# Optimization experiments

Hardware: AMD Instinct MI355X
Metric: run time of the kernel (lower is better)

## Reference

```python
import jax, jax.numpy as jnp
import numpy as np

HEADS = 8
WH, WW = 8, 8
DIM = 256
B = 4096
N = WH * WW  # 64


def _rel_index():
    ch, cw = np.meshgrid(np.arange(WH), np.arange(WW), indexing='ij')
    coords = np.stack([ch.ravel(), cw.ravel()])  # (2, N)
    rel = coords[:, :, None] - coords[:, None, :]  # (2, N, N)
    rel = rel.transpose(1, 2, 0)
    rel[:, :, 0] += WH - 1
    rel[:, :, 1] += WW - 1
    rel[:, :, 0] *= 2 * WW - 1
    return jnp.asarray(rel.sum(-1), dtype=jnp.int32)  # (N, N)


def setup_inputs() -> dict:
    key = jax.random.key(0)
    ks = jax.random.split(key, 6)
    x = jax.random.normal(ks[0], (B, N, DIM), dtype=jnp.float32)
    attn_mask = jnp.zeros((1, HEADS, N, N), dtype=jnp.float32)
    w_qkv = jax.random.normal(ks[1], (3 * DIM, DIM), dtype=jnp.float32) * 0.02
    w_proj = jax.random.normal(ks[2], (DIM, DIM), dtype=jnp.float32) * 0.02
    b_proj = jax.random.normal(ks[3], (DIM,), dtype=jnp.float32) * 0.02
    table = jax.random.normal(ks[4], (225, HEADS), dtype=jnp.float32) * 0.02
    return {"x": x, "attn_mask": attn_mask, "w_qkv": w_qkv, "w_proj": w_proj,
            "b_proj": b_proj, "table": table, "rel_index": _rel_index()}


def reference(x, attn_mask, w_qkv, w_proj, b_proj, table, rel_index):
    Bn, Nn, C = x.shape
    hd = C // HEADS
    qkv = (x @ w_qkv.T).reshape(Bn, Nn, 3, HEADS, hd)
    q = qkv[:, :, 0].transpose(0, 2, 1, 3)  # (B,h,N,d)
    k = qkv[:, :, 1].transpose(0, 2, 1, 3)
    v = qkv[:, :, 2].transpose(0, 2, 1, 3)
    scale = 1.0 / jnp.sqrt(jnp.asarray(hd, dtype=x.dtype))
    attn = jnp.einsum('bhnd,bhmd->bhnm', q, k) * scale
    bias = table[rel_index]  # (N,N,h)
    attn = attn + bias.transpose(2, 0, 1)[None] + attn_mask
    attn = jax.nn.softmax(attn, axis=-1)
    out = jnp.einsum('bhnm,bhmd->bhnd', attn, v)
    out = out.transpose(0, 2, 1, 3).reshape(Bn, Nn, C)
    return out @ w_proj.T + b_proj
```

## Files before the change

kernel.cpp:

```cpp
#include <hip/hip_runtime.h>
#include <hip/hip_bf16.h>

#define HEADS 8
#define NTOK 64
#define DIM 256

typedef __attribute__((ext_vector_type(8))) short bf16x8;
typedef __attribute__((ext_vector_type(4))) short bf16x4;
typedef __attribute__((ext_vector_type(4))) float f32x4;
typedef unsigned short u16;

__device__ __forceinline__ u16 f2bf(float f) {
    union { float f; unsigned u; } c; c.f = f;
    unsigned u = c.u;
    unsigned rounded = u + 0x7FFF + ((u >> 16) & 1);
    return (u16)(rounded >> 16);
}

__global__ void prep_kernel(const float* __restrict__ wqkv,
                            const float* __restrict__ wproj,
                            const float* __restrict__ table,
                            const int* __restrict__ rel_index,
                            const float* __restrict__ mask,
                            u16* __restrict__ wq_bf,
                            u16* __restrict__ wp_bf,
                            float* __restrict__ bias) {
    const int NQ = 768 * 256;
    const int NP = 256 * 256;
    const int NB = HEADS * NTOK * NTOK;
    int total = NQ + NP + NB;
    for (int i = blockIdx.x * blockDim.x + threadIdx.x; i < total;
         i += gridDim.x * blockDim.x) {
        if (i < NQ) {
            wq_bf[i] = f2bf(wqkv[i]);
        } else if (i < NQ + NP) {
            wp_bf[i - NQ] = f2bf(wproj[i - NQ]);
        } else {
            int j = i - (NQ + NP);
            int h = j >> 12;
            int nm = j & 4095;
            bias[j] = table[rel_index[nm] * HEADS + h] + mask[j];
        }
    }
}

__launch_bounds__(512, 2)
__global__ void win_attn_kernel(const float* __restrict__ x,
                                const u16* __restrict__ wq_bf,
                                const u16* __restrict__ wp_bf,
                                const float* __restrict__ bias,
                                const float* __restrict__ b_proj,
                                float* __restrict__ out) {
    __shared__ u16 smem[33792];
    u16* s_x = smem;
    u16* s_o = smem + 16896;

    const int b = blockIdx.x;
    const int tid = threadIdx.x;
    const int w = tid >> 6;
    const int l = tid & 63;
    const int l16 = l & 15;
    const int lhi = l >> 4;
    const int h = w;

    const u16* rq0 = wq_bf + (h * 32 + l16) * 256;
    const u16* rq1 = rq0 + 16 * 256;
    const u16* rk0 = wq_bf + (256 + h * 32 + l16) * 256;
    const u16* rk1 = rk0 + 16 * 256;
    const u16* rv0 = wq_bf + (512 + h * 32 + l16) * 256;
    const u16* rv1 = rv0 + 16 * 256;

    bf16x8 aq0 = *reinterpret_cast<const bf16x8*>(rq0 + lhi * 8);
    bf16x8 aq1 = *reinterpret_cast<const bf16x8*>(rq1 + lhi * 8);
    bf16x8 ak0 = *reinterpret_cast<const bf16x8*>(rk0 + lhi * 8);
    bf16x8 ak1 = *reinterpret_cast<const bf16x8*>(rk1 + lhi * 8);
    bf16x8 av0 = *reinterpret_cast<const bf16x8*>(rv0 + lhi * 8);
    bf16x8 av1 = *reinterpret_cast<const bf16x8*>(rv1 + lhi * 8);
    bf16x8 bq0 = *reinterpret_cast<const bf16x8*>(rq0 + 32 + lhi * 8);
    bf16x8 bq1 = *reinterpret_cast<const bf16x8*>(rq1 + 32 + lhi * 8);
    bf16x8 bk0 = *reinterpret_cast<const bf16x8*>(rk0 + 32 + lhi * 8);
    bf16x8 bk1 = *reinterpret_cast<const bf16x8*>(rk1 + 32 + lhi * 8);
    bf16x8 bv0 = *reinterpret_cast<const bf16x8*>(rv0 + 32 + lhi * 8);
    bf16x8 bv1 = *reinterpret_cast<const bf16x8*>(rv1 + 32 + lhi * 8);

    const float* xw = x + (size_t)b * (NTOK * DIM);
#pragma unroll
    for (int it = 0; it < 8; ++it) {
        int idx4 = tid + it * 512;
        float4 v = reinterpret_cast<const float4*>(xw)[idx4];
        int row = idx4 >> 6;
        int col = (idx4 & 63) * 4;
        ushort4 o;
        o.x = f2bf(v.x); o.y = f2bf(v.y); o.z = f2bf(v.z); o.w = f2bf(v.w);
        *reinterpret_cast<ushort4*>(&s_x[row * 264 + col]) = o;
    }
    __syncthreads();

    f32x4 qacc[2][4], kacc[2][4], vacc[4][2];
    const f32x4 zero = {0.f, 0.f, 0.f, 0.f};
#pragma unroll
    for (int ct = 0; ct < 2; ++ct)
#pragma unroll
        for (int tt = 0; tt < 4; ++tt) {
            qacc[ct][tt] = zero; kacc[ct][tt] = zero; vacc[tt][ct] = zero;
        }

    for (int ks = 0; ks < 8; ++ks) {
        const int k0 = ks * 32 + lhi * 8;
        bf16x8 xf[4];
#pragma unroll
        for (int tt = 0; tt < 4; ++tt)
            xf[tt] = *reinterpret_cast<const bf16x8*>(&s_x[(tt * 16 + l16) * 264 + k0]);
        bf16x8 nq0, nq1, nk0, nk1, nv0, nv1;
        if (ks < 6) {
            nq0 = *reinterpret_cast<const bf16x8*>(rq0 + k0 + 64);
            nq1 = *reinterpret_cast<const bf16x8*>(rq1 + k0 + 64);
            nk0 = *reinterpret_cast<const bf16x8*>(rk0 + k0 + 64);
            nk1 = *reinterpret_cast<const bf16x8*>(rk1 + k0 + 64);
            nv0 = *reinterpret_cast<const bf16x8*>(rv0 + k0 + 64);
            nv1 = *reinterpret_cast<const bf16x8*>(rv1 + k0 + 64);
        }
#pragma unroll
        for (int tt = 0; tt < 4; ++tt) {
            qacc[0][tt] = __builtin_amdgcn_mfma_f32_16x16x32_bf16(aq0, xf[tt], qacc[0][tt], 0, 0, 0);
            qacc[1][tt] = __builtin_amdgcn_mfma_f32_16x16x32_bf16(aq1, xf[tt], qacc[1][tt], 0, 0, 0);
            kacc[0][tt] = __builtin_amdgcn_mfma_f32_16x16x32_bf16(ak0, xf[tt], kacc[0][tt], 0, 0, 0);
            kacc[1][tt] = __builtin_amdgcn_mfma_f32_16x16x32_bf16(ak1, xf[tt], kacc[1][tt], 0, 0, 0);
            vacc[tt][0] = __builtin_amdgcn_mfma_f32_16x16x32_bf16(xf[tt], av0, vacc[tt][0], 0, 0, 0);
            vacc[tt][1] = __builtin_amdgcn_mfma_f32_16x16x32_bf16(xf[tt], av1, vacc[tt][1], 0, 0, 0);
        }
        aq0 = bq0; aq1 = bq1; ak0 = bk0; ak1 = bk1; av0 = bv0; av1 = bv1;
        bq0 = nq0; bq1 = nq1; bk0 = nk0; bk1 = nk1; bv0 = nv0; bv1 = nv1;
    }

    bf16x4 qf[4][2], kf[4][2], vf[4][2];
#pragma unroll
    for (int tt = 0; tt < 4; ++tt)
#pragma unroll
        for (int ct = 0; ct < 2; ++ct) {
            bf16x4 q, k, v;
#pragma unroll
            for (int r = 0; r < 4; ++r) {
                q[r] = (short)f2bf(qacc[ct][tt][r]);
                k[r] = (short)f2bf(kacc[ct][tt][r]);
                v[r] = (short)f2bf(vacc[tt][ct][r]);
            }
            qf[tt][ct] = q; kf[tt][ct] = k; vf[tt][ct] = v;
        }

    {
        const float scale = 0.17677669529663687f;
        const float* biash = bias + h * 4096;
        f32x4 bias_c[4], bias_n[4];
#pragma unroll
        for (int mt = 0; mt < 4; ++mt)
            bias_c[mt] = *reinterpret_cast<const f32x4*>(
                &biash[l16 * 64 + mt * 16 + lhi * 4]);

#pragma unroll
        for (int nt = 0; nt < 4; ++nt) {
            if (nt < 3) {
#pragma unroll
                for (int mt = 0; mt < 4; ++mt)
                    bias_n[mt] = *reinterpret_cast<const f32x4*>(
                        &biash[((nt + 1) * 16 + l16) * 64 + mt * 16 + lhi * 4]);
            }
            f32x4 sacc[4];
#pragma unroll
            for (int mt = 0; mt < 4; ++mt) {
                sacc[mt] = __builtin_amdgcn_mfma_f32_16x16x16bf16_1k(kf[mt][0], qf[nt][0], zero, 0, 0, 0);
                sacc[mt] = __builtin_amdgcn_mfma_f32_16x16x16bf16_1k(kf[mt][1], qf[nt][1], sacc[mt], 0, 0, 0);
            }
            float p[4][4];
            float sum = 0.f;
#pragma unroll
            for (int mt = 0; mt < 4; ++mt)
#pragma unroll
                for (int r = 0; r < 4; ++r) {
                    p[mt][r] = __expf(sacc[mt][r] * scale + bias_c[mt][r]);
                    sum += p[mt][r];
                }
            sum += __shfl_xor(sum, 16, 64);
            sum += __shfl_xor(sum, 32, 64);
            float inv = 1.0f / sum;
            bf16x4 pf[4];
#pragma unroll
            for (int mt = 0; mt < 4; ++mt) {
                bf16x4 pk;
#pragma unroll
                for (int r = 0; r < 4; ++r) pk[r] = (short)f2bf(p[mt][r]);
                pf[mt] = pk;
            }
            f32x4 oa0 = zero, oa1 = zero;
#pragma unroll
            for (int mt = 0; mt < 4; ++mt) {
                oa0 = __builtin_amdgcn_mfma_f32_16x16x16bf16_1k(vf[mt][0], pf[mt], oa0, 0, 0, 0);
                oa1 = __builtin_amdgcn_mfma_f32_16x16x16bf16_1k(vf[mt][1], pf[mt], oa1, 0, 0, 0);
            }
            {
                ushort4 o0, o1;
                o0.x = f2bf(oa0[0] * inv); o0.y = f2bf(oa0[1] * inv);
                o0.z = f2bf(oa0[2] * inv); o0.w = f2bf(oa0[3] * inv);
                o1.x = f2bf(oa1[0] * inv); o1.y = f2bf(oa1[1] * inv);
                o1.z = f2bf(oa1[2] * inv); o1.w = f2bf(oa1[3] * inv);
                u16* orow = &s_o[(nt * 16 + l16) * 264 + h * 32 + lhi * 4];
                *reinterpret_cast<ushort4*>(orow) = o0;
                *reinterpret_cast<ushort4*>(orow + 16) = o1;
            }
            if (nt < 3) {
#pragma unroll
                for (int mt = 0; mt < 4; ++mt) bias_c[mt] = bias_n[mt];
            }
        }
    }
    __syncthreads();

    f32x4 acc3[2][4];
#pragma unroll
    for (int t = 0; t < 2; ++t)
#pragma unroll
        for (int tt = 0; tt < 4; ++tt) acc3[t][tt] = zero;

    const u16* prow0 = wp_bf + (w * 16 + l16) * 256;
    const u16* prow1 = wp_bf + ((w + 8) * 16 + l16) * 256;
    bf16x8 wp0 = *reinterpret_cast<const bf16x8*>(prow0 + lhi * 8);
    bf16x8 wp1 = *reinterpret_cast<const bf16x8*>(prow1 + lhi * 8);
    for (int ks = 0; ks < 8; ++ks) {
        const int k0 = ks * 32 + lhi * 8;
        bf16x8 np0, np1;
        if (ks < 7) {
            np0 = *reinterpret_cast<const bf16x8*>(prow0 + k0 + 32);
            np1 = *reinterpret_cast<const bf16x8*>(prow1 + k0 + 32);
        }
#pragma unroll
        for (int tt = 0; tt < 4; ++tt) {
            bf16x8 of = *reinterpret_cast<const bf16x8*>(&s_o[(tt * 16 + l16) * 264 + k0]);
            acc3[0][tt] = __builtin_amdgcn_mfma_f32_16x16x32_bf16(wp0, of, acc3[0][tt], 0, 0, 0);
            acc3[1][tt] = __builtin_amdgcn_mfma_f32_16x16x32_bf16(wp1, of, acc3[1][tt], 0, 0, 0);
        }
        wp0 = np0; wp1 = np1;
    }
    float* outw = out + (size_t)b * (NTOK * DIM);
#pragma unroll
    for (int t = 0; t < 2; ++t) {
        int colb = (w + t * 8) * 16 + lhi * 4;
        float4 bp = *reinterpret_cast<const float4*>(&b_proj[colb]);
#pragma unroll
        for (int tt = 0; tt < 4; ++tt) {
            float4 o;
            o.x = acc3[t][tt][0] + bp.x;
            o.y = acc3[t][tt][1] + bp.y;
            o.z = acc3[t][tt][2] + bp.z;
            o.w = acc3[t][tt][3] + bp.w;
            *reinterpret_cast<float4*>(&outw[(tt * 16 + l16) * 256 + colb]) = o;
        }
    }
}

extern "C" void kernel_launch(void* const* d_in, const int* in_sizes, int n_in,
                              void* d_out, int out_size, void* d_ws, size_t ws_size,
                              hipStream_t stream) {
    const float* x     = (const float*)d_in[0];
    const float* mask  = (const float*)d_in[1];
    const float* wqkv  = (const float*)d_in[2];
    const float* wproj = (const float*)d_in[3];
    const float* bproj = (const float*)d_in[4];
    const float* table = (const float*)d_in[5];
    const int*   relix = (const int*)d_in[6];

    u16*   wq_bf = (u16*)d_ws;
    u16*   wp_bf = wq_bf + 768 * 256;
    float* bias  = (float*)(wp_bf + 256 * 256);

    prep_kernel<<<64, 512, 0, stream>>>(wqkv, wproj, table, relix, mask,
                                        wq_bf, wp_bf, bias);
    win_attn_kernel<<<4096, 512, 0, stream>>>(x, wq_bf, wp_bf, bias, bproj,
                                              (float*)d_out);
}
```

Measured before the change: 385.8 us.

## Halve block to 256 threads, loop each wave over two heads, repack attention output

The block shrinks from 8 to 4 waves, and each wave now handles two heads in sequence, so the per-head QKV, attention and PV code sits inside a two-iteration loop. The attention output in shared memory moves from a row-major 64x256 layout to per-head 64x36 tiles. The output projection then reads each head's tile as one K-slice and accumulates four output column tiles per wave. The aim is to amortize per-block setup and let more blocks share a CU, at the cost of more serial work per wave and slightly more shared memory.

```diff
diff --git a/kernel.cpp b/kernel.cpp
--- a/kernel.cpp
+++ b/kernel.cpp
@@ -44,14 +44,14 @@
     }
 }
 
-__launch_bounds__(512, 2)
+__launch_bounds__(256, 2)
 __global__ void win_attn_kernel(const float* __restrict__ x,
                                 const u16* __restrict__ wq_bf,
                                 const u16* __restrict__ wp_bf,
                                 const float* __restrict__ bias,
                                 const float* __restrict__ b_proj,
                                 float* __restrict__ out) {
-    __shared__ u16 smem[33792];
+    __shared__ u16 smem[35328];
     u16* s_x = smem;
     u16* s_o = smem + 16896;
 
@@ -61,32 +61,11 @@
     const int l = tid & 63;
     const int l16 = l & 15;
     const int lhi = l >> 4;
-    const int h = w;
-
-    const u16* rq0 = wq_bf + (h * 32 + l16) * 256;
-    const u16* rq1 = rq0 + 16 * 256;
-    const u16* rk0 = wq_bf + (256 + h * 32 + l16) * 256;
-    const u16* rk1 = rk0 + 16 * 256;
-    const u16* rv0 = wq_bf + (512 + h * 32 + l16) * 256;
-    const u16* rv1 = rv0 + 16 * 256;
-
-    bf16x8 aq0 = *reinterpret_cast<const bf16x8*>(rq0 + lhi * 8);
-    bf16x8 aq1 = *reinterpret_cast<const bf16x8*>(rq1 + lhi * 8);
-    bf16x8 ak0 = *reinterpret_cast<const bf16x8*>(rk0 + lhi * 8);
-    bf16x8 ak1 = *reinterpret_cast<const bf16x8*>(rk1 + lhi * 8);
-    bf16x8 av0 = *reinterpret_cast<const bf16x8*>(rv0 + lhi * 8);
-    bf16x8 av1 = *reinterpret_cast<const bf16x8*>(rv1 + lhi * 8);
-    bf16x8 bq0 = *reinterpret_cast<const bf16x8*>(rq0 + 32 + lhi * 8);
-    bf16x8 bq1 = *reinterpret_cast<const bf16x8*>(rq1 + 32 + lhi * 8);
-    bf16x8 bk0 = *reinterpret_cast<const bf16x8*>(rk0 + 32 + lhi * 8);
-    bf16x8 bk1 = *reinterpret_cast<const bf16x8*>(rk1 + 32 + lhi * 8);
-    bf16x8 bv0 = *reinterpret_cast<const bf16x8*>(rv0 + 32 + lhi * 8);
-    bf16x8 bv1 = *reinterpret_cast<const bf16x8*>(rv1 + 32 + lhi * 8);
 
     const float* xw = x + (size_t)b * (NTOK * DIM);
 #pragma unroll
-    for (int it = 0; it < 8; ++it) {
-        int idx4 = tid + it * 512;
+    for (int it = 0; it < 16; ++it) {
+        int idx4 = tid + it * 256;
         float4 v = reinterpret_cast<const float4*>(xw)[idx4];
         int row = idx4 >> 6;
         int col = (idx4 & 63) * 4;
@@ -96,60 +75,85 @@
     }
     __syncthreads();
 
-    f32x4 qacc[2][4], kacc[2][4], vacc[4][2];
     const f32x4 zero = {0.f, 0.f, 0.f, 0.f};
-#pragma unroll
-    for (int ct = 0; ct < 2; ++ct)
-#pragma unroll
-        for (int tt = 0; tt < 4; ++tt) {
-            qacc[ct][tt] = zero; kacc[ct][tt] = zero; vacc[tt][ct] = zero;
-        }
-
-    for (int ks = 0; ks < 8; ++ks) {
-        const int k0 = ks * 32 + lhi * 8;
-        bf16x8 xf[4];
+    const float scale = 0.17677669529663687f;
+
+#pragma unroll 1
+    for (int hh = 0; hh < 2; ++hh) {
+        const int h = w + hh * 4;
+
+        const u16* rq0 = wq_bf + (h * 32 + l16) * 256;
+        const u16* rq1 = rq0 + 16 * 256;
+        const u16* rk0 = wq_bf + (256 + h * 32 + l16) * 256;
+        const u16* rk1 = rk0 + 16 * 256;
+        const u16* rv0 = wq_bf + (512 + h * 32 + l16) * 256;
+        const u16* rv1 = rv0 + 16 * 256;
+
+        bf16x8 aq0 = *reinterpret_cast<const bf16x8*>(rq0 + lhi * 8);
+        bf16x8 aq1 = *reinterpret_cast<const bf16x8*>(rq1 + lhi * 8);
+        bf16x8 ak0 = *reinterpret_cast<const bf16x8*>(rk0 + lhi * 8);
+        bf16x8 ak1 = *reinterpret_cast<const bf16x8*>(rk1 + lhi * 8);
+        bf16x8 av0 = *reinterpret_cast<const bf16x8*>(rv0 + lhi * 8);
+        bf16x8 av1 = *reinterpret_cast<const bf16x8*>(rv1 + lhi * 8);
+        bf16x8 bq0 = *reinterpret_cast<const bf16x8*>(rq0 + 32 + lhi * 8);
+        bf16x8 bq1 = *reinterpret_cast<const bf16x8*>(rq1 + 32 + lhi * 8);
+        bf16x8 bk0 = *reinterpret_cast<const bf16x8*>(rk0 + 32 + lhi * 8);
+        bf16x8 bk1 = *reinterpret_cast<const bf16x8*>(rk1 + 32 + lhi * 8);
+        bf16x8 bv0 = *reinterpret_cast<const bf16x8*>(rv0 + 32 + lhi * 8);
+        bf16x8 bv1 = *reinterpret_cast<const bf16x8*>(rv1 + 32 + lhi * 8);
+
+        f32x4 qacc[2][4], kacc[2][4], vacc[4][2];
+#pragma unroll
+        for (int ct = 0; ct < 2; ++ct)
+#pragma unroll
+            for (int tt = 0; tt < 4; ++tt) {
+                qacc[ct][tt] = zero; kacc[ct][tt] = zero; vacc[tt][ct] = zero;
+            }
+
+        for (int ks = 0; ks < 8; ++ks) {
+            const int k0 = ks * 32 + lhi * 8;
+            bf16x8 xf[4];
+#pragma unroll
+            for (int tt = 0; tt < 4; ++tt)
+                xf[tt] = *reinterpret_cast<const bf16x8*>(&s_x[(tt * 16 + l16) * 264 + k0]);
+            bf16x8 nq0, nq1, nk0, nk1, nv0, nv1;
+            if (ks < 6) {
+                nq0 = *reinterpret_cast<const bf16x8*>(rq0 + k0 + 64);
+                nq1 = *reinterpret_cast<const bf16x8*>(rq1 + k0 + 64);
+                nk0 = *reinterpret_cast<const bf16x8*>(rk0 + k0 + 64);
+                nk1 = *reinterpret_cast<const bf16x8*>(rk1 + k0 + 64);
+                nv0 = *reinterpret_cast<const bf16x8*>(rv0 + k0 + 64);
+                nv1 = *reinterpret_cast<const bf16x8*>(rv1 + k0 + 64);
+            }
+#pragma unroll
+            for (int tt = 0; tt < 4; ++tt) {
+                qacc[0][tt] = __builtin_amdgcn_mfma_f32_16x16x32_bf16(aq0, xf[tt], qacc[0][tt], 0, 0, 0);
+                qacc[1][tt] = __builtin_amdgcn_mfma_f32_16x16x32_bf16(aq1, xf[tt], qacc[1][tt], 0, 0, 0);
+                kacc[0][tt] = __builtin_amdgcn_mfma_f32_16x16x32_bf16(ak0, xf[tt], kacc[0][tt], 0, 0, 0);
+                kacc[1][tt] = __builtin_amdgcn_mfma_f32_16x16x32_bf16(ak1, xf[tt], kacc[1][tt], 0, 0, 0);
+                vacc[tt][0] = __builtin_amdgcn_mfma_f32_16x16x32_bf16(xf[tt], av0, vacc[tt][0], 0, 0, 0);
+                vacc[tt][1] = __builtin_amdgcn_mfma_f32_16x16x32_bf16(xf[tt], av1, vacc[tt][1], 0, 0, 0);
+            }
+            aq0 = bq0; aq1 = bq1; ak0 = bk0; ak1 = bk1; av0 = bv0; av1 = bv1;
+            bq0 = nq0; bq1 = nq1; bk0 = nk0; bk1 = nk1; bv0 = nv0; bv1 = nv1;
+        }
+
+        bf16x4 qf[4][2], kf[4][2], vf[4][2];
 #pragma unroll
         for (int tt = 0; tt < 4; ++tt)
-            xf[tt] = *reinterpret_cast<const bf16x8*>(&s_x[(tt * 16 + l16) * 264 + k0]);
-        bf16x8 nq0, nq1, nk0, nk1, nv0, nv1;
-        if (ks < 6) {
-            nq0 = *reinterpret_cast<const bf16x8*>(rq0 + k0 + 64);
-            nq1 = *reinterpret_cast<const bf16x8*>(rq1 + k0 + 64);
-            nk0 = *reinterpret_cast<const bf16x8*>(rk0 + k0 + 64);
-            nk1 = *reinterpret_cast<const bf16x8*>(rk1 + k0 + 64);
-            nv0 = *reinterpret_cast<const bf16x8*>(rv0 + k0 + 64);
-            nv1 = *reinterpret_cast<const bf16x8*>(rv1 + k0 + 64);
-        }
-#pragma unroll
-        for (int tt = 0; tt < 4; ++tt) {
-            qacc[0][tt] = __builtin_amdgcn_mfma_f32_16x16x32_bf16(aq0, xf[tt], qacc[0][tt], 0, 0, 0);
-            qacc[1][tt] = __builtin_amdgcn_mfma_f32_16x16x32_bf16(aq1, xf[tt], qacc[1][tt], 0, 0, 0);
-            kacc[0][tt] = __builtin_amdgcn_mfma_f32_16x16x32_bf16(ak0, xf[tt], kacc[0][tt], 0, 0, 0);
-            kacc[1][tt] = __builtin_amdgcn_mfma_f32_16x16x32_bf16(ak1, xf[tt], kacc[1][tt], 0, 0, 0);
-            vacc[tt][0] = __builtin_amdgcn_mfma_f32_16x16x32_bf16(xf[tt], av0, vacc[tt][0], 0, 0, 0);
-            vacc[tt][1] = __builtin_amdgcn_mfma_f32_16x16x32_bf16(xf[tt], av1, vacc[tt][1], 0, 0, 0);
-        }
-        aq0 = bq0; aq1 = bq1; ak0 = bk0; ak1 = bk1; av0 = bv0; av1 = bv1;
-        bq0 = nq0; bq1 = nq1; bk0 = nk0; bk1 = nk1; bv0 = nv0; bv1 = nv1;
-    }
-
-    bf16x4 qf[4][2], kf[4][2], vf[4][2];
-#pragma unroll
-    for (int tt = 0; tt < 4; ++tt)
-#pragma unroll
-        for (int ct = 0; ct < 2; ++ct) {
-            bf16x4 q, k, v;
-#pragma unroll
-            for (int r = 0; r < 4; ++r) {
-                q[r] = (short)f2bf(qacc[ct][tt][r]);
-                k[r] = (short)f2bf(kacc[ct][tt][r]);
-                v[r] = (short)f2bf(vacc[tt][ct][r]);
-            }
-            qf[tt][ct] = q; kf[tt][ct] = k; vf[tt][ct] = v;
-        }
-
-    {
-        const float scale = 0.17677669529663687f;
+#pragma unroll
+            for (int ct = 0; ct < 2; ++ct) {
+                bf16x4 q, k, v;
+#pragma unroll
+                for (int r = 0; r < 4; ++r) {
+                    q[r] = (short)f2bf(qacc[ct][tt][r]);
+                    k[r] = (short)f2bf(kacc[ct][tt][r]);
+                    v[r] = (short)f2bf(vacc[tt][ct][r]);
+                }
+                qf[tt][ct] = q; kf[tt][ct] = k; vf[tt][ct] = v;
+            }
+
+        u16* Oh = s_o + h * 2304;
         const float* biash = bias + h * 4096;
         f32x4 bias_c[4], bias_n[4];
 #pragma unroll
@@ -203,7 +207,7 @@
                 o0.z = f2bf(oa0[2] * inv); o0.w = f2bf(oa0[3] * inv);
                 o1.x = f2bf(oa1[0] * inv); o1.y = f2bf(oa1[1] * inv);
                 o1.z = f2bf(oa1[2] * inv); o1.w = f2bf(oa1[3] * inv);
-                u16* orow = &s_o[(nt * 16 + l16) * 264 + h * 32 + lhi * 4];
+                u16* orow = &Oh[(nt * 16 + l16) * 36 + lhi * 4];
                 *reinterpret_cast<ushort4*>(orow) = o0;
                 *reinterpret_cast<ushort4*>(orow + 16) = o1;
             }
@@ -215,35 +219,42 @@
     }
     __syncthreads();
 
-    f32x4 acc3[2][4];
-#pragma unroll
-    for (int t = 0; t < 2; ++t)
+    f32x4 acc3[4][4];
+#pragma unroll
+    for (int t = 0; t < 4; ++t)
 #pragma unroll
         for (int tt = 0; tt < 4; ++tt) acc3[t][tt] = zero;
 
-    const u16* prow0 = wp_bf + (w * 16 + l16) * 256;
-    const u16* prow1 = wp_bf + ((w + 8) * 16 + l16) * 256;
-    bf16x8 wp0 = *reinterpret_cast<const bf16x8*>(prow0 + lhi * 8);
-    bf16x8 wp1 = *reinterpret_cast<const bf16x8*>(prow1 + lhi * 8);
+    const u16* prow[4];
+    bf16x8 wpc[4], wpn[4];
+#pragma unroll
+    for (int t = 0; t < 4; ++t) {
+        prow[t] = wp_bf + ((w + 4 * t) * 16 + l16) * 256;
+        wpc[t] = *reinterpret_cast<const bf16x8*>(prow[t] + lhi * 8);
+    }
     for (int ks = 0; ks < 8; ++ks) {
-        const int k0 = ks * 32 + lhi * 8;
-        bf16x8 np0, np1;
         if (ks < 7) {
-            np0 = *reinterpret_cast<const bf16x8*>(prow0 + k0 + 32);
-            np1 = *reinterpret_cast<const bf16x8*>(prow1 + k0 + 32);
-        }
+            const int k0n = (ks + 1) * 32 + lhi * 8;
+#pragma unroll
+            for (int t = 0; t < 4; ++t)
+                wpn[t] = *reinterpret_cast<const bf16x8*>(prow[t] + k0n);
+        }
+        const u16* Ohk = s_o + ks * 2304;
 #pragma unroll
         for (int tt = 0; tt < 4; ++tt) {
-            bf16x8 of = *reinterpret_cast<const bf16x8*>(&s_o[(tt * 16 + l16) * 264 + k0]);
-            acc3[0][tt] = __builtin_amdgcn_mfma_f32_16x16x32_bf16(wp0, of, acc3[0][tt], 0, 0, 0);
-            acc3[1][tt] = __builtin_amdgcn_mfma_f32_16x16x32_bf16(wp1, of, acc3[1][tt], 0, 0, 0);
-        }
-        wp0 = np0; wp1 = np1;
+            bf16x8 of = *reinterpret_cast<const bf16x8*>(
+                &Ohk[(tt * 16 + l16) * 36 + lhi * 8]);
+#pragma unroll
+            for (int t = 0; t < 4; ++t)
+                acc3[t][tt] = __builtin_amdgcn_mfma_f32_16x16x32_bf16(wpc[t], of, acc3[t][tt], 0, 0, 0);
+        }
+#pragma unroll
+        for (int t = 0; t < 4; ++t) wpc[t] = wpn[t];
     }
     float* outw = out + (size_t)b * (NTOK * DIM);
 #pragma unroll
-    for (int t = 0; t < 2; ++t) {
-        int colb = (w + t * 8) * 16 + lhi * 4;
+    for (int t = 0; t < 4; ++t) {
+        int colb = (w + 4 * t) * 16 + lhi * 4;
         float4 bp = *reinterpret_cast<const float4*>(&b_proj[colb]);
 #pragma unroll
         for (int tt = 0; tt < 4; ++tt) {
@@ -274,6 +285,6 @@
 
     prep_kernel<<<64, 512, 0, stream>>>(wqkv, wproj, table, relix, mask,
                                         wq_bf, wp_bf, bias);
-    win_attn_kernel<<<4096, 512, 0, stream>>>(x, wq_bf, wp_bf, bias, bproj,
+    win_attn_kernel<<<4096, 256, 0, stream>>>(x, wq_bf, wp_bf, bias, bproj,
                                               (float*)d_out);
 }
```

Measured after the change: 451.7 us. 17.1% more time.
